# Kernel optimization log

Measured on AMD Instinct MI355X. Metric: run time of the kernel, lower is better.

Reference implementation:

```python
import jax, jax.numpy as jnp
import numpy as np

NC_MEM = 64          # nTemporalMemoryChannels
NC_IMG = 64          # nImageFeatureChannels
FTL_RATIO = 0.5      # temporalFTLRatio
N_BLOCKS = 3         # nTemporalBlocks
B, H, W = 32, 64, 96
M = 32               # memory buffer length (= max(memory_idx)+1)


def setup_inputs() -> dict:
    key = jax.random.key(0)
    ks = jax.random.split(key, 8)
    eye = jnp.eye(4, dtype=jnp.float32)
    img_features = jax.random.normal(ks[0], (B, NC_IMG, H, W), jnp.float32)
    prev_mem_features = jax.random.normal(ks[1], (M, NC_MEM, H, W), jnp.float32)
    # extrinsics: random perturbation around identity so torch.inverse-equivalent is well conditioned
    prev_extrinsics = 0.1 * jax.random.normal(ks[2], (M, 4, 4), jnp.float32) + eye
    cur_extrinsics = 0.1 * jax.random.normal(ks[3], (B, 4, 4), jnp.float32) + eye
    memory_idx = jnp.arange(B, dtype=jnp.int32)
    use_memory = jax.random.randint(ks[4], (B,), 0, 2).astype(bool)
    NC = NC_MEM + NC_IMG
    Ws = jax.random.normal(ks[5], (N_BLOCKS, NC, NC), jnp.float32) * (1.0 / np.sqrt(NC))
    bs = jax.random.normal(ks[6], (N_BLOCKS, NC), jnp.float32) * 0.01
    return {
        "img_features": img_features,
        "prev_mem_features": prev_mem_features,
        "prev_extrinsics": prev_extrinsics,
        "cur_extrinsics": cur_extrinsics,
        "memory_idx": memory_idx,
        "use_memory": use_memory,
        "Ws": Ws,
        "bs": bs,
    }


def _apply_ftl(xf, feats, ratio):
    # Feature Transform Layer: first `ratio` fraction of channels (rounded down
    # to a multiple of 4) treated as groups of homogeneous 4-vectors per pixel,
    # warped by the 4x4 transform xf; remaining channels pass through.
    b, c, h, w = feats.shape
    nc_ftl = (int(c * ratio) // 4) * 4
    g = nc_ftl // 4
    pts = feats[:, :nc_ftl].reshape(b, g, 4, h * w)
    pts = jnp.einsum("bij,bgjp->bgip", xf, pts).reshape(b, nc_ftl, h, w)
    return jnp.concatenate([pts, feats[:, nc_ftl:]], axis=1)


def reference(img_features, prev_mem_features, prev_extrinsics, cur_extrinsics,
              memory_idx, use_memory, Ws, bs):
    eye = jnp.eye(4, dtype=prev_extrinsics.dtype)
    # --- transform_memory_features (gather + extrinsics warp, masked) ---
    mem_g = prev_mem_features[memory_idx]              # [B, NC_MEM, H, W]
    prev_ext_g = prev_extrinsics[memory_idx]           # [B, 4, 4]
    # entries with use_memory=False are zeroed; guard inverse with identity
    safe_prev = jnp.where(use_memory[:, None, None], prev_ext_g, eye)
    prev_cam0_to_world = jnp.linalg.inv(safe_prev)
    xf = jnp.einsum("bij,bjk->bik", cur_extrinsics, prev_cam0_to_world)
    mem_xfed = _apply_ftl(xf, mem_g, FTL_RATIO)
    mem_xfed = jnp.where(use_memory[:, None, None, None], mem_xfed,
                         jnp.zeros((), mem_xfed.dtype))
    # --- forward_one_step: concat + 1x1 conv stack (pointwise matmuls) ---
    x = jnp.concatenate([mem_xfed, img_features], axis=1)  # [B, 128, H, W]
    n = Ws.shape[0]
    for i in range(n):
        x = jnp.einsum("oc,bchw->bohw", Ws[i], x) + bs[i][None, :, None, None]
        if i != n - 1:
            x = jax.nn.relu(x)
    fused_features = x[:, NC_MEM:]                     # returned output
    return fused_features
```

## Files before the change

kernel.cpp:

```cpp
#include <hip/hip_runtime.h>
#include <hip/hip_fp16.h>

#define NC_MEM 64
#define NC_IMG 64
#define NC     128
#define B_     32
#define H_     64
#define W_     96
#define HW_    (H_ * W_)
#define P_TILE 64
#define NTILES (HW_ / P_TILE)
#define FS     520
#define FOFF(pt, ks) ((((pt) * 4) + (ks)) * FS)
#define XOFF(pt, ks, blk) (FOFF(pt, ks) + ((((blk) + (pt)) & 63) << 3))

#define WA_HI  0
#define WA_LO  98304
#define XF_OFF 196608
#define UM_OFF 198656

typedef _Float16 f16x8 __attribute__((ext_vector_type(8)));
typedef __attribute__((ext_vector_type(4))) float f32x4;

__device__ inline unsigned pk2h(float a, float b) {
    __half2 h = __floats2half2_rn(a, b);
    return *(const unsigned*)&h;
}

__device__ inline void bar_lds() {
    __builtin_amdgcn_sched_barrier(0);
    asm volatile("s_waitcnt lgkmcnt(0)" ::: "memory");
    __builtin_amdgcn_s_barrier();
    asm volatile("" ::: "memory");
    __builtin_amdgcn_sched_barrier(0);
}

__global__ void prep(const float* __restrict__ Ws,
                     const float* __restrict__ prev_ext,
                     const float* __restrict__ cur_ext,
                     const int* __restrict__ mem_idx,
                     const unsigned char* __restrict__ um_raw,
                     unsigned char* __restrict__ wsb) {
    if (blockIdx.x < 192) {
        int idx = blockIdx.x * 256 + threadIdx.x;
        int l = idx >> 14, r = idx & 16383, o = r >> 7, c = r & 127;
        float w = Ws[idx];
        __half hi = __float2half_rn(w);
        __half lo = __float2half_rn(w - __half2float(hi));
        int mt = o >> 4, lm = o & 15, ks = c >> 5, kr = c & 31, q = kr >> 3, j = kr & 7;
        int lane = q * 16 + lm;
        int di = ((((l * 8 + mt) * 4 + ks) * 64 + lane) << 3) + j;
        ((unsigned short*)(wsb + WA_HI))[di] = __half_as_ushort(hi);
        ((unsigned short*)(wsb + WA_LO))[di] = __half_as_ushort(lo);
        return;
    }
    int tb = threadIdx.x;
    if (tb >= 64) return;
    bool flag = (tb < 32) && (tb & 3) && (um_raw[tb] != 0);
    bool is_bool = __any(flag);
    if (tb >= B_) return;
    int b = tb;
    bool um = is_bool ? (um_raw[b] != 0) : (((const int*)um_raw)[b] != 0);
    int mi = mem_idx[b];

    float a[16];
#pragma unroll
    for (int i = 0; i < 16; ++i)
        a[i] = um ? prev_ext[mi * 16 + i] : ((i % 5 == 0) ? 1.f : 0.f);

    float s0 = a[0]*a[5]  - a[1]*a[4];
    float s1 = a[0]*a[6]  - a[2]*a[4];
    float s2 = a[0]*a[7]  - a[3]*a[4];
    float s3 = a[1]*a[6]  - a[2]*a[5];
    float s4 = a[1]*a[7]  - a[3]*a[5];
    float s5 = a[2]*a[7]  - a[3]*a[6];
    float c5 = a[10]*a[15] - a[11]*a[14];
    float c4 = a[9]*a[15]  - a[11]*a[13];
    float c3 = a[9]*a[14]  - a[10]*a[13];
    float c2 = a[8]*a[15]  - a[11]*a[12];
    float c1 = a[8]*a[14]  - a[10]*a[12];
    float c0 = a[8]*a[13]  - a[9]*a[12];
    float det = s0*c5 - s1*c4 + s2*c3 + s3*c2 - s4*c1 + s5*c0;
    float id = 1.0f / det;

    float inv[16];
    inv[0]  = ( a[5]*c5  - a[6]*c4  + a[7]*c3)  * id;
    inv[1]  = (-a[1]*c5  + a[2]*c4  - a[3]*c3)  * id;
    inv[2]  = ( a[13]*s5 - a[14]*s4 + a[15]*s3) * id;
    inv[3]  = (-a[9]*s5  + a[10]*s4 - a[11]*s3) * id;
    inv[4]  = (-a[4]*c5  + a[6]*c2  - a[7]*c1)  * id;
    inv[5]  = ( a[0]*c5  - a[2]*c2  + a[3]*c1)  * id;
    inv[6]  = (-a[12]*s5 + a[14]*s2 - a[15]*s1) * id;
    inv[7]  = ( a[8]*s5  - a[10]*s2 + a[11]*s1) * id;
    inv[8]  = ( a[4]*c4  - a[5]*c2  + a[7]*c0)  * id;
    inv[9]  = (-a[0]*c4  + a[1]*c2  - a[3]*c0)  * id;
    inv[10] = ( a[12]*s4 - a[13]*s2 + a[15]*s0) * id;
    inv[11] = (-a[8]*s4  + a[9]*s2  - a[11]*s0) * id;
    inv[12] = (-a[4]*c3  + a[5]*c1  - a[6]*c0)  * id;
    inv[13] = ( a[0]*c3  - a[1]*c1  + a[2]*c0)  * id;
    inv[14] = (-a[12]*s3 + a[13]*s1 - a[14]*s0) * id;
    inv[15] = ( a[8]*s3  - a[9]*s1  + a[10]*s0) * id;

    float* xf = (float*)(wsb + XF_OFF) + b * 16;
#pragma unroll
    for (int i = 0; i < 4; ++i)
#pragma unroll
        for (int j2 = 0; j2 < 4; ++j2) {
            float s = 0.f;
#pragma unroll
            for (int k = 0; k < 4; ++k)
                s += cur_ext[b * 16 + i * 4 + k] * inv[k * 4 + j2];
            xf[i * 4 + j2] = s;
        }
    ((float*)(wsb + UM_OFF))[b] = um ? 1.f : 0.f;
}

__global__ __launch_bounds__(256, 4)
void fused_main(const float* __restrict__ img, const float* __restrict__ mem,
                const int* __restrict__ mem_idx, const float* __restrict__ bs,
                const unsigned char* __restrict__ wsb, float* __restrict__ out) {
    __shared__ unsigned short xh[16 * FS];

    const int t   = threadIdx.x;
    const int b   = blockIdx.y;
    const int hw0 = blockIdx.x * P_TILE;
    const bool umb = ((const float*)(wsb + UM_OFF))[b] != 0.f;
    const int mi  = mem_idx[b];

    const f16x8* __restrict__ WH = (const f16x8*)(wsb + WA_HI);
    const f16x8* __restrict__ WL = (const f16x8*)(wsb + WA_LO);

    const int w    = t >> 6;
    const int lane = t & 63;
    const int wq   = lane >> 4;
    const int lm   = lane & 15;
    const int mt0  = 2 * w;
    const int mt2  = 4 + w;

#define FI(l, mt, ks) (((((l) * 8 + (mt)) * 4) + (ks)) * 64 + lane)

    {
        const int q   = t & 15;
        const int og  = t >> 4;
        const int px0 = hw0 + q * 4;
        const int pt  = q >> 2;
        if (umb) {
            const int c0 = og * 8;
            const float* basep = (c0 < NC_MEM)
                ? (mem + ((size_t)mi * NC_MEM + c0) * HW_ + px0)
                : (img + ((size_t)b * NC_IMG + (c0 - NC_MEM)) * HW_ + px0);
            f32x4 v[8];
#pragma unroll
            for (int cc = 0; cc < 8; ++cc)
                v[cc] = *(const f32x4*)(basep + (size_t)cc * HW_);
            if (og < 4) {
                float xfv[16];
                const float* xfp = (const float*)(wsb + XF_OFF) + b * 16;
#pragma unroll
                for (int j = 0; j < 4; ++j)
                    *(f32x4*)&xfv[j * 4] = *(const f32x4*)&xfp[j * 4];
#pragma unroll
                for (int sg = 0; sg < 2; ++sg) {
#pragma unroll
                    for (int i = 0; i < 4; ++i) {
                        float a0 = v[4*sg+0][i], a1 = v[4*sg+1][i];
                        float a2 = v[4*sg+2][i], a3 = v[4*sg+3][i];
                        v[4*sg+0][i] = xfv[0]*a0  + xfv[1]*a1  + xfv[2]*a2  + xfv[3]*a3;
                        v[4*sg+1][i] = xfv[4]*a0  + xfv[5]*a1  + xfv[6]*a2  + xfv[7]*a3;
                        v[4*sg+2][i] = xfv[8]*a0  + xfv[9]*a1  + xfv[10]*a2 + xfv[11]*a3;
                        v[4*sg+3][i] = xfv[12]*a0 + xfv[13]*a1 + xfv[14]*a2 + xfv[15]*a3;
                    }
                }
            }
            const int bk0 = (og & 3) * 16 + (q & 3) * 4;
#pragma unroll
            for (int i = 0; i < 4; ++i) {
                uint4 pk;
                pk.x = pk2h(v[0][i], v[1][i]);
                pk.y = pk2h(v[2][i], v[3][i]);
                pk.z = pk2h(v[4][i], v[5][i]);
                pk.w = pk2h(v[6][i], v[7][i]);
                *(uint4*)&xh[XOFF(pt, og >> 2, bk0 + i)] = pk;
            }
        } else {
            const int gg = 16 + og;
            const int c0 = gg * 4 - NC_MEM;
            f32x4 u[4];
#pragma unroll
            for (int cc = 0; cc < 4; ++cc)
                u[cc] = *(const f32x4*)(img + ((size_t)b * NC_IMG + c0 + cc) * HW_ + px0);
            const int bk0 = ((gg & 7) >> 1) * 16 + (q & 3) * 4;
            const int hoff = (gg & 1) * 4;
#pragma unroll
            for (int i = 0; i < 4; ++i)
                *(uint2*)&xh[XOFF(pt, gg >> 3, bk0 + i) + hoff] =
                    make_uint2(pk2h(u[0][i], u[1][i]), pk2h(u[2][i], u[3][i]));
        }
    }

    const unsigned short* bp[4];
#pragma unroll
    for (int nt = 0; nt < 4; ++nt)
        bp[nt] = &xh[XOFF(nt, 0, lane)];

    const int kpa = umb ? 0 : 2, kpb = umb ? 1 : 3;
    f16x8 p0h = WH[FI(0, mt0,     kpa)], p0l = WL[FI(0, mt0,     kpa)];
    f16x8 p1h = WH[FI(0, mt0 + 1, kpa)], p1l = WL[FI(0, mt0 + 1, kpa)];
    f16x8 p2h = WH[FI(0, mt0,     kpb)], p2l = WL[FI(0, mt0,     kpb)];
    f16x8 p3h = WH[FI(0, mt0 + 1, kpb)], p3l = WL[FI(0, mt0 + 1, kpb)];

    bar_lds();

    f32x4 acc[2][4];

    auto run_ks = [&](int ks, f16x8 ah0, f16x8 al0, f16x8 ah1, f16x8 al1) {
#pragma unroll
        for (int nt = 0; nt < 4; ++nt) {
            f16x8 bh = *(const f16x8*)(bp[nt] + ks * FS);
            acc[0][nt] = __builtin_amdgcn_mfma_f32_16x16x32_f16(ah0, bh, acc[0][nt], 0, 0, 0);
            acc[1][nt] = __builtin_amdgcn_mfma_f32_16x16x32_f16(ah1, bh, acc[1][nt], 0, 0, 0);
            acc[0][nt] = __builtin_amdgcn_mfma_f32_16x16x32_f16(al0, bh, acc[0][nt], 0, 0, 0);
            acc[1][nt] = __builtin_amdgcn_mfma_f32_16x16x32_f16(al1, bh, acc[1][nt], 0, 0, 0);
        }
    };
    auto writeback = [&]() {
#pragma unroll
        for (int mi2 = 0; mi2 < 2; ++mi2) {
            const int mt = mt0 + mi2;
            const int ks2 = mt >> 1;
            const int lane_f = ((mt & 1) * 2 + (wq >> 1)) * 16 + lm;
            const int j0 = (wq & 1) * 4;
#pragma unroll
            for (int nt = 0; nt < 4; ++nt) {
                float v0 = fmaxf(acc[mi2][nt][0], 0.f);
                float v1 = fmaxf(acc[mi2][nt][1], 0.f);
                float v2 = fmaxf(acc[mi2][nt][2], 0.f);
                float v3 = fmaxf(acc[mi2][nt][3], 0.f);
                *(uint2*)&xh[XOFF(nt, ks2, lane_f) + j0] =
                    make_uint2(pk2h(v0, v1), pk2h(v2, v3));
            }
        }
    };

#pragma unroll
    for (int mi2 = 0; mi2 < 2; ++mi2) {
        f32x4 bv = *(const f32x4*)&bs[0 * NC + (mt0 + mi2) * 16 + wq * 4];
#pragma unroll
        for (int nt = 0; nt < 4; ++nt) acc[mi2][nt] = bv;
    }
    __builtin_amdgcn_s_setprio(1);
    if (umb) {
        run_ks(0, p0h, p0l, p1h, p1l);
        run_ks(1, p2h, p2l, p3h, p3l);
        run_ks(2, WH[FI(0, mt0, 2)], WL[FI(0, mt0, 2)],
                  WH[FI(0, mt0 + 1, 2)], WL[FI(0, mt0 + 1, 2)]);
        run_ks(3, WH[FI(0, mt0, 3)], WL[FI(0, mt0, 3)],
                  WH[FI(0, mt0 + 1, 3)], WL[FI(0, mt0 + 1, 3)]);
    } else {
        run_ks(2, p0h, p0l, p1h, p1l);
        run_ks(3, p2h, p2l, p3h, p3l);
    }
    __builtin_amdgcn_s_setprio(0);
    f16x8 q0h = WH[FI(1, mt0, 0)],     q0l = WL[FI(1, mt0, 0)];
    f16x8 q1h = WH[FI(1, mt0 + 1, 0)], q1l = WL[FI(1, mt0 + 1, 0)];
    f16x8 q2h = WH[FI(1, mt0, 1)],     q2l = WL[FI(1, mt0, 1)];
    f16x8 q3h = WH[FI(1, mt0 + 1, 1)], q3l = WL[FI(1, mt0 + 1, 1)];
    bar_lds();
    writeback();
    bar_lds();

#pragma unroll
    for (int mi2 = 0; mi2 < 2; ++mi2) {
        f32x4 bv = *(const f32x4*)&bs[1 * NC + (mt0 + mi2) * 16 + wq * 4];
#pragma unroll
        for (int nt = 0; nt < 4; ++nt) acc[mi2][nt] = bv;
    }
    __builtin_amdgcn_s_setprio(1);
    run_ks(0, q0h, q0l, q1h, q1l);
    run_ks(1, q2h, q2l, q3h, q3l);
    run_ks(2, WH[FI(1, mt0, 2)], WL[FI(1, mt0, 2)],
              WH[FI(1, mt0 + 1, 2)], WL[FI(1, mt0 + 1, 2)]);
    run_ks(3, WH[FI(1, mt0, 3)], WL[FI(1, mt0, 3)],
              WH[FI(1, mt0 + 1, 3)], WL[FI(1, mt0 + 1, 3)]);
    __builtin_amdgcn_s_setprio(0);
    f16x8 r0h = WH[FI(2, mt2, 0)], r0l = WL[FI(2, mt2, 0)];
    f16x8 r1h = WH[FI(2, mt2, 1)], r1l = WL[FI(2, mt2, 1)];
    f16x8 r2h = WH[FI(2, mt2, 2)], r2l = WL[FI(2, mt2, 2)];
    f16x8 r3h = WH[FI(2, mt2, 3)], r3l = WL[FI(2, mt2, 3)];
    bar_lds();
    writeback();
    bar_lds();

    {
        f32x4 a2[4];
        f32x4 bv = *(const f32x4*)&bs[2 * NC + mt2 * 16 + wq * 4];
#pragma unroll
        for (int nt = 0; nt < 4; ++nt) a2[nt] = bv;
        auto run2 = [&](int ks, f16x8 ah, f16x8 al) {
#pragma unroll
            for (int nt = 0; nt < 4; ++nt) {
                f16x8 bh = *(const f16x8*)(bp[nt] + ks * FS);
                a2[nt] = __builtin_amdgcn_mfma_f32_16x16x32_f16(ah, bh, a2[nt], 0, 0, 0);
                a2[nt] = __builtin_amdgcn_mfma_f32_16x16x32_f16(al, bh, a2[nt], 0, 0, 0);
            }
        };
        __builtin_amdgcn_s_setprio(1);
        run2(0, r0h, r0l);
        run2(1, r1h, r1l);
        run2(2, r2h, r2l);
        run2(3, r3h, r3l);
        __builtin_amdgcn_s_setprio(0);
        const int oc0 = mt2 * 16 + wq * 4 - 64;
#pragma unroll
        for (int nt = 0; nt < 4; ++nt) {
            float* dst = out + ((size_t)b * 64 + oc0) * HW_ + hw0 + nt * 16 + lm;
#pragma unroll
            for (int r = 0; r < 4; ++r)
                __builtin_nontemporal_store(a2[nt][r], dst + (size_t)r * HW_);
        }
    }
#undef FI
}

extern "C" void kernel_launch(void* const* d_in, const int* in_sizes, int n_in,
                              void* d_out, int out_size, void* d_ws, size_t ws_size,
                              hipStream_t stream) {
    const float* img  = (const float*)d_in[0];
    const float* mem  = (const float*)d_in[1];
    const float* pext = (const float*)d_in[2];
    const float* cext = (const float*)d_in[3];
    const int*   midx = (const int*)d_in[4];
    const unsigned char* umem = (const unsigned char*)d_in[5];
    const float* Ws   = (const float*)d_in[6];
    const float* bs   = (const float*)d_in[7];
    float* out = (float*)d_out;
    unsigned char* wsb = (unsigned char*)d_ws;

    hipLaunchKernelGGL(prep, dim3(193), dim3(256), 0, stream,
                       Ws, pext, cext, midx, umem, wsb);
    hipLaunchKernelGGL(fused_main, dim3(NTILES, B_), dim3(256), 0, stream,
                       img, mem, midx, bs, wsb, out);
}
```

Before: 160.7 us.

## Fuse prep kernel into main: inline weight split and extrinsic inverse

Removes the separate prep launch. Each block now loads fp32 weights directly and splits them into fp16 hi/lo in registers, and recomputes the 4x4 inverse and transform per thread. The launch bound drops from 4 to 3 waves per SIMD. This removes one kernel launch and a workspace round trip, at the cost of redundant conversion and inverse arithmetic in every block, uncoalesced fp32 weight loads, and possibly lower occupancy.

After: 184.5 us. 1.15x slower.

```diff
diff --git a/kernel.cpp b/kernel.cpp
--- a/kernel.cpp
+++ b/kernel.cpp
@@ -14,17 +14,29 @@
 #define FOFF(pt, ks) ((((pt) * 4) + (ks)) * FS)
 #define XOFF(pt, ks, blk) (FOFF(pt, ks) + ((((blk) + (pt)) & 63) << 3))
 
-#define WA_HI  0
-#define WA_LO  98304
-#define XF_OFF 196608
-#define UM_OFF 198656
-
 typedef _Float16 f16x8 __attribute__((ext_vector_type(8)));
 typedef __attribute__((ext_vector_type(4))) float f32x4;
+
+struct w8 { f32x4 a, b; };
 
 __device__ inline unsigned pk2h(float a, float b) {
     __half2 h = __floats2half2_rn(a, b);
     return *(const unsigned*)&h;
+}
+
+__device__ inline w8 ldw(const float* __restrict__ Ws, int l, int mt, int ks, int lane) {
+    const float* s = Ws + (((size_t)(l * 128 + mt * 16 + (lane & 15))) * 128
+                           + ks * 32 + ((lane >> 4) << 3));
+    w8 r; r.a = *(const f32x4*)s; r.b = *(const f32x4*)(s + 4); return r;
+}
+__device__ inline void cvtw(const w8& w, f16x8& hi, f16x8& lo) {
+#pragma unroll
+    for (int j = 0; j < 8; ++j) {
+        float x = (j < 4) ? w.a[j] : w.b[j - 4];
+        _Float16 h = (_Float16)x;
+        hi[j] = h;
+        lo[j] = (_Float16)(x - (float)h);
+    }
 }
 
 __device__ inline void bar_lds() {
@@ -35,100 +47,18 @@
     __builtin_amdgcn_sched_barrier(0);
 }
 
-__global__ void prep(const float* __restrict__ Ws,
-                     const float* __restrict__ prev_ext,
-                     const float* __restrict__ cur_ext,
-                     const int* __restrict__ mem_idx,
-                     const unsigned char* __restrict__ um_raw,
-                     unsigned char* __restrict__ wsb) {
-    if (blockIdx.x < 192) {
-        int idx = blockIdx.x * 256 + threadIdx.x;
-        int l = idx >> 14, r = idx & 16383, o = r >> 7, c = r & 127;
-        float w = Ws[idx];
-        __half hi = __float2half_rn(w);
-        __half lo = __float2half_rn(w - __half2float(hi));
-        int mt = o >> 4, lm = o & 15, ks = c >> 5, kr = c & 31, q = kr >> 3, j = kr & 7;
-        int lane = q * 16 + lm;
-        int di = ((((l * 8 + mt) * 4 + ks) * 64 + lane) << 3) + j;
-        ((unsigned short*)(wsb + WA_HI))[di] = __half_as_ushort(hi);
-        ((unsigned short*)(wsb + WA_LO))[di] = __half_as_ushort(lo);
-        return;
-    }
-    int tb = threadIdx.x;
-    if (tb >= 64) return;
-    bool flag = (tb < 32) && (tb & 3) && (um_raw[tb] != 0);
-    bool is_bool = __any(flag);
-    if (tb >= B_) return;
-    int b = tb;
-    bool um = is_bool ? (um_raw[b] != 0) : (((const int*)um_raw)[b] != 0);
-    int mi = mem_idx[b];
-
-    float a[16];
-#pragma unroll
-    for (int i = 0; i < 16; ++i)
-        a[i] = um ? prev_ext[mi * 16 + i] : ((i % 5 == 0) ? 1.f : 0.f);
-
-    float s0 = a[0]*a[5]  - a[1]*a[4];
-    float s1 = a[0]*a[6]  - a[2]*a[4];
-    float s2 = a[0]*a[7]  - a[3]*a[4];
-    float s3 = a[1]*a[6]  - a[2]*a[5];
-    float s4 = a[1]*a[7]  - a[3]*a[5];
-    float s5 = a[2]*a[7]  - a[3]*a[6];
-    float c5 = a[10]*a[15] - a[11]*a[14];
-    float c4 = a[9]*a[15]  - a[11]*a[13];
-    float c3 = a[9]*a[14]  - a[10]*a[13];
-    float c2 = a[8]*a[15]  - a[11]*a[12];
-    float c1 = a[8]*a[14]  - a[10]*a[12];
-    float c0 = a[8]*a[13]  - a[9]*a[12];
-    float det = s0*c5 - s1*c4 + s2*c3 + s3*c2 - s4*c1 + s5*c0;
-    float id = 1.0f / det;
-
-    float inv[16];
-    inv[0]  = ( a[5]*c5  - a[6]*c4  + a[7]*c3)  * id;
-    inv[1]  = (-a[1]*c5  + a[2]*c4  - a[3]*c3)  * id;
-    inv[2]  = ( a[13]*s5 - a[14]*s4 + a[15]*s3) * id;
-    inv[3]  = (-a[9]*s5  + a[10]*s4 - a[11]*s3) * id;
-    inv[4]  = (-a[4]*c5  + a[6]*c2  - a[7]*c1)  * id;
-    inv[5]  = ( a[0]*c5  - a[2]*c2  + a[3]*c1)  * id;
-    inv[6]  = (-a[12]*s5 + a[14]*s2 - a[15]*s1) * id;
-    inv[7]  = ( a[8]*s5  - a[10]*s2 + a[11]*s1) * id;
-    inv[8]  = ( a[4]*c4  - a[5]*c2  + a[7]*c0)  * id;
-    inv[9]  = (-a[0]*c4  + a[1]*c2  - a[3]*c0)  * id;
-    inv[10] = ( a[12]*s4 - a[13]*s2 + a[15]*s0) * id;
-    inv[11] = (-a[8]*s4  + a[9]*s2  - a[11]*s0) * id;
-    inv[12] = (-a[4]*c3  + a[5]*c1  - a[6]*c0)  * id;
-    inv[13] = ( a[0]*c3  - a[1]*c1  + a[2]*c0)  * id;
-    inv[14] = (-a[12]*s3 + a[13]*s1 - a[14]*s0) * id;
-    inv[15] = ( a[8]*s3  - a[9]*s1  + a[10]*s0) * id;
-
-    float* xf = (float*)(wsb + XF_OFF) + b * 16;
-#pragma unroll
-    for (int i = 0; i < 4; ++i)
-#pragma unroll
-        for (int j2 = 0; j2 < 4; ++j2) {
-            float s = 0.f;
-#pragma unroll
-            for (int k = 0; k < 4; ++k)
-                s += cur_ext[b * 16 + i * 4 + k] * inv[k * 4 + j2];
-            xf[i * 4 + j2] = s;
-        }
-    ((float*)(wsb + UM_OFF))[b] = um ? 1.f : 0.f;
-}
-
-__global__ __launch_bounds__(256, 4)
+__global__ __launch_bounds__(256, 3)
 void fused_main(const float* __restrict__ img, const float* __restrict__ mem,
                 const int* __restrict__ mem_idx, const float* __restrict__ bs,
-                const unsigned char* __restrict__ wsb, float* __restrict__ out) {
+                const float* __restrict__ Ws,
+                const float* __restrict__ prev_ext, const float* __restrict__ cur_ext,
+                const unsigned char* __restrict__ um_raw,
+                float* __restrict__ out) {
     __shared__ unsigned short xh[16 * FS];
 
     const int t   = threadIdx.x;
     const int b   = blockIdx.y;
     const int hw0 = blockIdx.x * P_TILE;
-    const bool umb = ((const float*)(wsb + UM_OFF))[b] != 0.f;
-    const int mi  = mem_idx[b];
-
-    const f16x8* __restrict__ WH = (const f16x8*)(wsb + WA_HI);
-    const f16x8* __restrict__ WL = (const f16x8*)(wsb + WA_LO);
 
     const int w    = t >> 6;
     const int lane = t & 63;
@@ -137,7 +67,10 @@
     const int mt0  = 2 * w;
     const int mt2  = 4 + w;
 
-#define FI(l, mt, ks) (((((l) * 8 + (mt)) * 4) + (ks)) * 64 + lane)
+    const int mi = mem_idx[b];
+    bool flag = (lane < 32) && (lane & 3) && (um_raw[lane] != 0);
+    bool is_bool = __any(flag);
+    const bool umb = is_bool ? (um_raw[b] != 0) : (((const int*)um_raw)[b] != 0);
 
     {
         const int q   = t & 15;
@@ -154,11 +87,56 @@
             for (int cc = 0; cc < 8; ++cc)
                 v[cc] = *(const f32x4*)(basep + (size_t)cc * HW_);
             if (og < 4) {
+                float a[16], cv[16];
+                const float* pe = prev_ext + (size_t)mi * 16;
+                const float* ce = cur_ext + (size_t)b * 16;
+#pragma unroll
+                for (int j = 0; j < 4; ++j) {
+                    *(f32x4*)&a[j * 4]  = *(const f32x4*)(pe + j * 4);
+                    *(f32x4*)&cv[j * 4] = *(const f32x4*)(ce + j * 4);
+                }
+                float s0 = a[0]*a[5]  - a[1]*a[4];
+                float s1 = a[0]*a[6]  - a[2]*a[4];
+                float s2 = a[0]*a[7]  - a[3]*a[4];
+                float s3 = a[1]*a[6]  - a[2]*a[5];
+                float s4 = a[1]*a[7]  - a[3]*a[5];
+                float s5 = a[2]*a[7]  - a[3]*a[6];
+                float c5 = a[10]*a[15] - a[11]*a[14];
+                float c4 = a[9]*a[15]  - a[11]*a[13];
+                float c3 = a[9]*a[14]  - a[10]*a[13];
+                float c2 = a[8]*a[15]  - a[11]*a[12];
+                float c1 = a[8]*a[14]  - a[10]*a[12];
+                float c0f = a[8]*a[13] - a[9]*a[12];
+                float det = s0*c5 - s1*c4 + s2*c3 + s3*c2 - s4*c1 + s5*c0f;
+                float id = 1.0f / det;
+                float inv[16];
+                inv[0]  = ( a[5]*c5  - a[6]*c4  + a[7]*c3)  * id;
+                inv[1]  = (-a[1]*c5  + a[2]*c4  - a[3]*c3)  * id;
+                inv[2]  = ( a[13]*s5 - a[14]*s4 + a[15]*s3) * id;
+                inv[3]  = (-a[9]*s5  + a[10]*s4 - a[11]*s3) * id;
+                inv[4]  = (-a[4]*c5  + a[6]*c2  - a[7]*c1)  * id;
+                inv[5]  = ( a[0]*c5  - a[2]*c2  + a[3]*c1)  * id;
+                inv[6]  = (-a[12]*s5 + a[14]*s2 - a[15]*s1) * id;
+                inv[7]  = ( a[8]*s5  - a[10]*s2 + a[11]*s1) * id;
+                inv[8]  = ( a[4]*c4  - a[5]*c2  + a[7]*c0f) * id;
+                inv[9]  = (-a[0]*c4  + a[1]*c2  - a[3]*c0f) * id;
+                inv[10] = ( a[12]*s4 - a[13]*s2 + a[15]*s0) * id;
+                inv[11] = (-a[8]*s4  + a[9]*s2  - a[11]*s0) * id;
+                inv[12] = (-a[4]*c3  + a[5]*c1  - a[6]*c0f) * id;
+                inv[13] = ( a[0]*c3  - a[1]*c1  + a[2]*c0f) * id;
+                inv[14] = (-a[12]*s3 + a[13]*s1 - a[14]*s0) * id;
+                inv[15] = ( a[8]*s3  - a[9]*s1  + a[10]*s0) * id;
                 float xfv[16];
-                const float* xfp = (const float*)(wsb + XF_OFF) + b * 16;
-#pragma unroll
-                for (int j = 0; j < 4; ++j)
-                    *(f32x4*)&xfv[j * 4] = *(const f32x4*)&xfp[j * 4];
+#pragma unroll
+                for (int i = 0; i < 4; ++i)
+#pragma unroll
+                    for (int j2 = 0; j2 < 4; ++j2) {
+                        float s = 0.f;
+#pragma unroll
+                        for (int k = 0; k < 4; ++k)
+                            s += cv[i * 4 + k] * inv[k * 4 + j2];
+                        xfv[i * 4 + j2] = s;
+                    }
 #pragma unroll
                 for (int sg = 0; sg < 2; ++sg) {
 #pragma unroll
@@ -204,10 +182,10 @@
         bp[nt] = &xh[XOFF(nt, 0, lane)];
 
     const int kpa = umb ? 0 : 2, kpb = umb ? 1 : 3;
-    f16x8 p0h = WH[FI(0, mt0,     kpa)], p0l = WL[FI(0, mt0,     kpa)];
-    f16x8 p1h = WH[FI(0, mt0 + 1, kpa)], p1l = WL[FI(0, mt0 + 1, kpa)];
-    f16x8 p2h = WH[FI(0, mt0,     kpb)], p2l = WL[FI(0, mt0,     kpb)];
-    f16x8 p3h = WH[FI(0, mt0 + 1, kpb)], p3l = WL[FI(0, mt0 + 1, kpb)];
+    w8 pw0 = ldw(Ws, 0, mt0,     kpa, lane);
+    w8 pw1 = ldw(Ws, 0, mt0 + 1, kpa, lane);
+    w8 pw2 = ldw(Ws, 0, mt0,     kpb, lane);
+    w8 pw3 = ldw(Ws, 0, mt0 + 1, kpb, lane);
 
     bar_lds();
 
@@ -222,6 +200,12 @@
             acc[0][nt] = __builtin_amdgcn_mfma_f32_16x16x32_f16(al0, bh, acc[0][nt], 0, 0, 0);
             acc[1][nt] = __builtin_amdgcn_mfma_f32_16x16x32_f16(al1, bh, acc[1][nt], 0, 0, 0);
         }
+    };
+    auto run_ks_w = [&](int l, int ks) {
+        w8 wa = ldw(Ws, l, mt0, ks, lane), wb = ldw(Ws, l, mt0 + 1, ks, lane);
+        f16x8 ah0, al0, ah1, al1;
+        cvtw(wa, ah0, al0); cvtw(wb, ah1, al1);
+        run_ks(ks, ah0, al0, ah1, al1);
     };
     auto writeback = [&]() {
 #pragma unroll
@@ -248,23 +232,24 @@
 #pragma unroll
         for (int nt = 0; nt < 4; ++nt) acc[mi2][nt] = bv;
     }
-    __builtin_amdgcn_s_setprio(1);
-    if (umb) {
-        run_ks(0, p0h, p0l, p1h, p1l);
-        run_ks(1, p2h, p2l, p3h, p3l);
-        run_ks(2, WH[FI(0, mt0, 2)], WL[FI(0, mt0, 2)],
-                  WH[FI(0, mt0 + 1, 2)], WL[FI(0, mt0 + 1, 2)]);
-        run_ks(3, WH[FI(0, mt0, 3)], WL[FI(0, mt0, 3)],
-                  WH[FI(0, mt0 + 1, 3)], WL[FI(0, mt0 + 1, 3)]);
-    } else {
-        run_ks(2, p0h, p0l, p1h, p1l);
-        run_ks(3, p2h, p2l, p3h, p3l);
-    }
-    __builtin_amdgcn_s_setprio(0);
-    f16x8 q0h = WH[FI(1, mt0, 0)],     q0l = WL[FI(1, mt0, 0)];
-    f16x8 q1h = WH[FI(1, mt0 + 1, 0)], q1l = WL[FI(1, mt0 + 1, 0)];
-    f16x8 q2h = WH[FI(1, mt0, 1)],     q2l = WL[FI(1, mt0, 1)];
-    f16x8 q3h = WH[FI(1, mt0 + 1, 1)], q3l = WL[FI(1, mt0 + 1, 1)];
+    {
+        f16x8 p0h, p0l, p1h, p1l, p2h, p2l, p3h, p3l;
+        cvtw(pw0, p0h, p0l); cvtw(pw1, p1h, p1l);
+        cvtw(pw2, p2h, p2l); cvtw(pw3, p3h, p3l);
+        __builtin_amdgcn_s_setprio(1);
+        if (umb) {
+            run_ks(0, p0h, p0l, p1h, p1l);
+            run_ks(1, p2h, p2l, p3h, p3l);
+            run_ks_w(0, 2);
+            run_ks_w(0, 3);
+        } else {
+            run_ks(2, p0h, p0l, p1h, p1l);
+            run_ks(3, p2h, p2l, p3h, p3l);
+        }
+        __builtin_amdgcn_s_setprio(0);
+    }
+    w8 qw0 = ldw(Ws, 1, mt0, 0, lane), qw1 = ldw(Ws, 1, mt0 + 1, 0, lane);
+    w8 qw2 = ldw(Ws, 1, mt0, 1, lane), qw3 = ldw(Ws, 1, mt0 + 1, 1, lane);
     bar_lds();
     writeback();
     bar_lds();
@@ -275,18 +260,19 @@
 #pragma unroll
         for (int nt = 0; nt < 4; ++nt) acc[mi2][nt] = bv;
     }
-    __builtin_amdgcn_s_setprio(1);
-    run_ks(0, q0h, q0l, q1h, q1l);
-    run_ks(1, q2h, q2l, q3h, q3l);
-    run_ks(2, WH[FI(1, mt0, 2)], WL[FI(1, mt0, 2)],
-              WH[FI(1, mt0 + 1, 2)], WL[FI(1, mt0 + 1, 2)]);
-    run_ks(3, WH[FI(1, mt0, 3)], WL[FI(1, mt0, 3)],
-              WH[FI(1, mt0 + 1, 3)], WL[FI(1, mt0 + 1, 3)]);
-    __builtin_amdgcn_s_setprio(0);
-    f16x8 r0h = WH[FI(2, mt2, 0)], r0l = WL[FI(2, mt2, 0)];
-    f16x8 r1h = WH[FI(2, mt2, 1)], r1l = WL[FI(2, mt2, 1)];
-    f16x8 r2h = WH[FI(2, mt2, 2)], r2l = WL[FI(2, mt2, 2)];
-    f16x8 r3h = WH[FI(2, mt2, 3)], r3l = WL[FI(2, mt2, 3)];
+    {
+        f16x8 q0h, q0l, q1h, q1l, q2h, q2l, q3h, q3l;
+        cvtw(qw0, q0h, q0l); cvtw(qw1, q1h, q1l);
+        cvtw(qw2, q2h, q2l); cvtw(qw3, q3h, q3l);
+        __builtin_amdgcn_s_setprio(1);
+        run_ks(0, q0h, q0l, q1h, q1l);
+        run_ks(1, q2h, q2l, q3h, q3l);
+        run_ks_w(1, 2);
+        run_ks_w(1, 3);
+        __builtin_amdgcn_s_setprio(0);
+    }
+    w8 rw0 = ldw(Ws, 2, mt2, 0, lane), rw1 = ldw(Ws, 2, mt2, 1, lane);
+    w8 rw2 = ldw(Ws, 2, mt2, 2, lane), rw3 = ldw(Ws, 2, mt2, 3, lane);
     bar_lds();
     writeback();
     bar_lds();
@@ -304,6 +290,9 @@
                 a2[nt] = __builtin_amdgcn_mfma_f32_16x16x32_f16(al, bh, a2[nt], 0, 0, 0);
             }
         };
+        f16x8 r0h, r0l, r1h, r1l, r2h, r2l, r3h, r3l;
+        cvtw(rw0, r0h, r0l); cvtw(rw1, r1h, r1l);
+        cvtw(rw2, r2h, r2l); cvtw(rw3, r3h, r3l);
         __builtin_amdgcn_s_setprio(1);
         run2(0, r0h, r0l);
         run2(1, r1h, r1l);
@@ -319,7 +308,6 @@
                 __builtin_nontemporal_store(a2[nt][r], dst + (size_t)r * HW_);
         }
     }
-#undef FI
 }
 
 extern "C" void kernel_launch(void* const* d_in, const int* in_sizes, int n_in,
@@ -334,10 +322,8 @@
     const float* Ws   = (const float*)d_in[6];
     const float* bs   = (const float*)d_in[7];
     float* out = (float*)d_out;
-    unsigned char* wsb = (unsigned char*)d_ws;
-
-    hipLaunchKernelGGL(prep, dim3(193), dim3(256), 0, stream,
-                       Ws, pext, cext, midx, umem, wsb);
+    (void)d_ws; (void)ws_size;
+
     hipLaunchKernelGGL(fused_main, dim3(NTILES, B_), dim3(256), 0, stream,
-                       img, mem, midx, bs, wsb, out);
-}
+                       img, mem, midx, bs, Ws, pext, cext, umem, out);
+}
```
